# Kernel tuning notes

Hardware: AMD Instinct MI355X
Metric: run time of the kernel (lower is better)

Reference implementation:

```python
import jax, jax.numpy as jnp
import numpy as np

N = 100000   # nodes
E = 300000   # edges
D = 256      # emb_dim
L = 5        # num_layers
SELF_LOOP_BOND_TYPE = 4
BN_EPS = 1e-5


def setup_inputs() -> dict:
    key = jax.random.key(0)
    ks = jax.random.split(key, 12)
    s = 0.05
    x = jax.random.randint(ks[0], (N, 2), 0, 3)
    edge_index = jax.random.randint(ks[1], (2, E), 0, N)
    edge_attr = jax.random.randint(ks[2], (E, 2), 0, 3)
    x_emb1 = jax.random.normal(ks[3], (120, D), dtype=jnp.float32) * s
    x_emb2 = jax.random.normal(ks[4], (3, D), dtype=jnp.float32) * s
    edge_emb1 = jax.random.normal(ks[5], (L, 6, D), dtype=jnp.float32) * s
    edge_emb2 = jax.random.normal(ks[6], (L, 3, D), dtype=jnp.float32) * s
    W1 = jax.random.normal(ks[7], (L, D, 2 * D), dtype=jnp.float32) * (1.0 / np.sqrt(D))
    b1 = jnp.zeros((L, 2 * D), dtype=jnp.float32)
    W2 = jax.random.normal(ks[8], (L, 2 * D, D), dtype=jnp.float32) * (1.0 / np.sqrt(2 * D))
    b2 = jnp.zeros((L, D), dtype=jnp.float32)
    bn_gamma = jnp.ones((L - 1, D), dtype=jnp.float32)
    bn_beta = jnp.zeros((L - 1, D), dtype=jnp.float32)
    return dict(x=x, edge_index=edge_index, edge_attr=edge_attr,
                x_emb1=x_emb1, x_emb2=x_emb2,
                edge_emb1=edge_emb1, edge_emb2=edge_emb2,
                W1=W1, b1=b1, W2=W2, b2=b2,
                bn_gamma=bn_gamma, bn_beta=bn_beta)


def reference(x, edge_index, edge_attr, x_emb1, x_emb2, edge_emb1, edge_emb2,
              W1, b1, W2, b2, bn_gamma, bn_beta):
    n = x.shape[0]
    loop = jnp.arange(n)
    # add_self_loops: append (i, i) for every node
    src = jnp.concatenate([edge_index[0], loop])  # [E+N]
    dst = jnp.concatenate([edge_index[1], loop])  # [E+N]
    # self-loop edge_attr = (bond_type=4, direction=0)
    self_attr = jnp.concatenate([
        jnp.full((n, 1), SELF_LOOP_BOND_TYPE, dtype=edge_attr.dtype),
        jnp.zeros((n, 1), dtype=edge_attr.dtype)], axis=1)
    ea = jnp.concatenate([edge_attr, self_attr], axis=0)  # [E+N, 2]

    out = x_emb1[x[:, 0]] + x_emb2[x[:, 1]]  # [N, D]
    for l in range(L):
        e_emb = edge_emb1[l][ea[:, 0]] + edge_emb2[l][ea[:, 1]]  # [E+N, D]
        msg = out[src] + e_emb                                   # gather + message
        agg = jax.ops.segment_sum(msg, dst, num_segments=n)      # scatter-add
        h = jax.nn.relu(agg @ W1[l] + b1[l]) @ W2[l] + b2[l]     # GIN MLP
        if l < L - 1:
            mean = h.mean(axis=0)
            var = h.var(axis=0)  # biased var, matches torch BN training
            h = (h - mean) * jax.lax.rsqrt(var + BN_EPS) * bn_gamma[l] + bn_beta[l]
            h = jax.nn.relu(h)
        out = h
    return out
```

## Files before the change

### kernel.cpp

```cpp
#include <hip/hip_runtime.h>

typedef unsigned short u16;
typedef unsigned int u32;

#define DD 256

typedef short  s16x8 __attribute__((ext_vector_type(8)));
typedef short  s16x4 __attribute__((ext_vector_type(4)));
typedef float  f32x4 __attribute__((ext_vector_type(4)));

__device__ __forceinline__ float b2f(u16 u){
  union { u32 i; float f; } c; c.i = ((u32)u) << 16; return c.f;
}
__device__ __forceinline__ u16 f2b(float f){
  union { float f; u32 i; } c; c.f = f;
  u32 b = c.i + 0x7FFFu + ((c.i >> 16) & 1u);
  return (u16)(b >> 16);
}

__global__ void NodeEncoder_72971494359603_kernel(){}

__global__ void probe_dtype(const u32* w, u32* flag){
  if (threadIdx.x == 0 && blockIdx.x == 0){
    int cnt = 0;
    for (int i = 0; i < 256; i++){
      u32 low = w[i] & 0xFFFFu;
      u32 e = (low >> 7) & 0xFFu;
      if (e >= 0x60u && e <= 0x7Eu) cnt++;
    }
    *flag = (cnt >= 192) ? 1u : 0u;
  }
}

__global__ void cvt_in(const void* src, u16* dst, int n, const u32* flag){
  int i = blockIdx.x * 256 + threadIdx.x;
  if (i < n){
    if (*flag){
      dst[i] = ((const u16*)src)[i];
    } else {
      dst[i] = f2b(((const float*)src)[i]);
    }
  }
}

__global__ void store_out(const u16* h, void* dout, int n, const u32* flag){
  int i = blockIdx.x * 256 + threadIdx.x;
  if (i < n){
    if (*flag){
      ((u16*)dout)[i] = h[i];
    } else {
      ((float*)dout)[i] = b2f(h[i]);
    }
  }
}

__global__ void zero_int(int* p, int n){
  int i = blockIdx.x * 256 + threadIdx.x;
  if (i < n) p[i] = 0;
}

__global__ void build_table(const u16* ee1, const u16* ee2, u16* TBL){
  int b = blockIdx.x;
  int l = b / 18, c = b % 18, a = c / 3, bb = c % 3;
  int j = threadIdx.x;
  TBL[b * DD + j] = f2b(b2f(ee1[(l * 6 + a) * DD + j]) + b2f(ee2[(l * 3 + bb) * DD + j]));
}

__global__ void hist_kernel(const int* dst, int* counts, int E){
  int e = blockIdx.x * 256 + threadIdx.x;
  if (e < E) atomicAdd(&counts[dst[e]], 1);
}

__global__ void scan_sums(const int* counts, int* bsum, int N){
  __shared__ int red[256];
  int tid = threadIdx.x;
  int base = blockIdx.x * 1024;
  int s = 0;
  for (int i = tid; i < 1024; i += 256){
    int g = base + i;
    if (g < N) s += counts[g];
  }
  red[tid] = s;
  __syncthreads();
  for (int off = 128; off > 0; off >>= 1){
    if (tid < off) red[tid] += red[tid + off];
    __syncthreads();
  }
  if (tid == 0) bsum[blockIdx.x] = red[0];
}

__global__ void scan_top(int* bsum, int nb){
  if (threadIdx.x == 0 && blockIdx.x == 0){
    int acc = 0;
    for (int i = 0; i < nb; i++){ int t = bsum[i]; bsum[i] = acc; acc += t; }
  }
}

__global__ void scan_block(const int* counts, const int* bsum,
                           int* offsets, int* cursor, int N){
  __shared__ int tsum[256];
  int b = blockIdx.x;
  int tid = threadIdx.x;
  int base = b * 1024;
  int v0, v1, v2, v3;
  int g = base + tid * 4;
  v0 = (g + 0 < N) ? counts[g + 0] : 0;
  v1 = (g + 1 < N) ? counts[g + 1] : 0;
  v2 = (g + 2 < N) ? counts[g + 2] : 0;
  v3 = (g + 3 < N) ? counts[g + 3] : 0;
  tsum[tid] = v0 + v1 + v2 + v3;
  __syncthreads();
  for (int off = 1; off < 256; off <<= 1){
    int t = (tid >= off) ? tsum[tid - off] : 0;
    __syncthreads();
    tsum[tid] += t;
    __syncthreads();
  }
  int excl = (tid == 0 ? 0 : tsum[tid - 1]) + bsum[b];
  if (g + 0 < N){ offsets[g + 0] = excl; cursor[g + 0] = excl; } excl += v0;
  if (g + 1 < N){ offsets[g + 1] = excl; cursor[g + 1] = excl; } excl += v1;
  if (g + 2 < N){ offsets[g + 2] = excl; cursor[g + 2] = excl; } excl += v2;
  if (g + 3 < N){ offsets[g + 3] = excl; cursor[g + 3] = excl; }
}

__global__ void fill_csr(const int* ei, const int* ea, int* cursor,
                         int* payload, int E){
  int e = blockIdx.x * 256 + threadIdx.x;
  if (e < E){
    int d = ei[E + e];
    int pos = atomicAdd(&cursor[d], 1);
    int a = ea[2 * e], bb = ea[2 * e + 1];
    payload[pos] = ei[e] | ((a * 3 + bb) << 17);
  }
}

__global__ void node_embed(const int* x, const u16* xe1, const u16* xe2,
                           u16* out, int N){
  int idx = blockIdx.x * 256 + threadIdx.x;
  if (idx < N * DD){
    int n = idx >> 8, j = idx & 255;
    int x0 = x[2 * n], x1 = x[2 * n + 1];
    out[idx] = f2b(b2f(xe1[x0 * DD + j]) + b2f(xe2[x1 * DD + j]));
  }
}

__global__ void pack_B(const u16* __restrict__ W0, u16* __restrict__ Wp0, int K, int Nc){
  const u16* W = W0 + (size_t)blockIdx.y * K * Nc;
  u16* Wp = Wp0 + (size_t)blockIdx.y * K * Nc;
  int idx = blockIdx.x * 256 + threadIdx.x;
  int lane = idx & 63;
  int t = idx >> 6;
  int nk = K >> 5;
  int ksub = t % nk, cblk = t / nk;
  if (cblk >= (Nc >> 4)) return;
  int col = cblk * 16 + (lane & 15);
  int krow = ksub * 32 + (lane >> 4) * 8;
  u16* dst = Wp + (size_t)idx * 8;
#pragma unroll
  for (int e = 0; e < 8; e++)
    dst[e] = W[(size_t)(krow + e) * Nc + col];
}

__global__ __launch_bounds__(512, 6)
void layer_fused(const u16* __restrict__ feat, const u16* __restrict__ TBL,
                 const int* __restrict__ offsets, const int* __restrict__ counts,
                 const int* __restrict__ payload,
                 const u16* __restrict__ Wp1, const u16* __restrict__ bias1,
                 const u16* __restrict__ Wp2, const u16* __restrict__ bias2,
                 u16* __restrict__ H, float* __restrict__ partial, int npart, int M,
                 const float* __restrict__ sums, const u16* __restrict__ gamma,
                 const u16* __restrict__ beta, float invN, int apply_bn){
  __shared__ __align__(16) u16 As[64 * 256];
  __shared__ __align__(16) u16 Ms[2][64 * 64];
  u16* T = (u16*)Ms;
  int tid = threadIdx.x, lane = tid & 63, wave = tid >> 6;
  int wr = wave >> 2, wc = wave & 3;
  int row0 = blockIdx.x * 64;
  int lr = lane & 15, hi = lane >> 4;

  {
    u32* Tw = (u32*)T;
    const u32* Gw = (const u32*)TBL;
    for (int i = tid; i < 18 * DD / 2; i += 512) Tw[i] = Gw[i];
  }
  __syncthreads();

  {
    int c4 = lane * 4;
    float sc[4], sh[4];
    if (apply_bn){
#pragma unroll
      for (int e = 0; e < 4; e++){
        int j = c4 + e;
        float mean = sums[j] * invN;
        float var = sums[DD + j] * invN - mean * mean;
        if (var < 0.f) var = 0.f;
        float scl = rsqrtf(var + 1e-5f) * b2f(gamma[j]);
        sc[e] = scl; sh[e] = b2f(beta[j]) - mean * scl;
      }
    } else {
#pragma unroll
      for (int e = 0; e < 4; e++){ sc[e] = 1.f; sh[e] = 0.f; }
    }
    for (int u = 0; u < 8; u++){
      int r = wave * 8 + u;
      int n = row0 + r; if (n > M - 1) n = M - 1;
      s16x4 sv = *(const s16x4*)(feat + (size_t)n * DD + c4);
      s16x4 tb = *(const s16x4*)(T + 12 * DD + c4);
      float v0 = b2f((u16)sv[0]) * sc[0] + sh[0];
      float v1 = b2f((u16)sv[1]) * sc[1] + sh[1];
      float v2 = b2f((u16)sv[2]) * sc[2] + sh[2];
      float v3 = b2f((u16)sv[3]) * sc[3] + sh[3];
      if (apply_bn){
        v0 = fmaxf(v0, 0.f); v1 = fmaxf(v1, 0.f);
        v2 = fmaxf(v2, 0.f); v3 = fmaxf(v3, 0.f);
      }
      float a0 = v0 + b2f((u16)tb[0]);
      float a1 = v1 + b2f((u16)tb[1]);
      float a2 = v2 + b2f((u16)tb[2]);
      float a3 = v3 + b2f((u16)tb[3]);
      int e0 = offsets[n], eend = e0 + counts[n];
      for (int e = e0; e < eend; e += 4){
        int nb = eend - e; if (nb > 4) nb = 4;
        int pls[4]; s16x4 rvs[4]; s16x4 tvs[4];
#pragma unroll
        for (int i = 0; i < 4; i++)
          if (i < nb) pls[i] = payload[e + i];
#pragma unroll
        for (int i = 0; i < 4; i++)
          if (i < nb){
            rvs[i] = *(const s16x4*)(feat + (size_t)(pls[i] & 0x1FFFF) * DD + c4);
            tvs[i] = *(const s16x4*)(T + (pls[i] >> 17) * DD + c4);
          }
#pragma unroll
        for (int i = 0; i < 4; i++)
          if (i < nb){
            float w0 = b2f((u16)rvs[i][0]) * sc[0] + sh[0];
            float w1 = b2f((u16)rvs[i][1]) * sc[1] + sh[1];
            float w2 = b2f((u16)rvs[i][2]) * sc[2] + sh[2];
            float w3 = b2f((u16)rvs[i][3]) * sc[3] + sh[3];
            if (apply_bn){
              w0 = fmaxf(w0, 0.f); w1 = fmaxf(w1, 0.f);
              w2 = fmaxf(w2, 0.f); w3 = fmaxf(w3, 0.f);
            }
            a0 += w0 + b2f((u16)tvs[i][0]);
            a1 += w1 + b2f((u16)tvs[i][1]);
            a2 += w2 + b2f((u16)tvs[i][2]);
            a3 += w3 + b2f((u16)tvs[i][3]);
          }
      }
      s16x4 o;
      o[0] = (short)f2b(a0); o[1] = (short)f2b(a1);
      o[2] = (short)f2b(a2); o[3] = (short)f2b(a3);
      int byteo = r * 512 + ((((lane >> 1) ^ (r & 7)) & 31) << 4) + ((lane & 1) << 3);
      *(s16x4*)((char*)As + byteo) = o;
    }
  }
  __syncthreads();

  f32x4 zero = {0.f, 0.f, 0.f, 0.f};
  f32x4 acc2[2][4];
#pragma unroll
  for (int m = 0; m < 2; m++)
#pragma unroll
    for (int n = 0; n < 4; n++) acc2[m][n] = zero;
  f32x4 acc1[2];

  auto G1 = [&](int cc){
    acc1[0] = zero; acc1[1] = zero;
    int cb = cc * 4 + wc;
#pragma unroll
    for (int ks = 0; ks < 8; ks++){
      s16x8 af[2];
#pragma unroll
      for (int m = 0; m < 2; m++){
        int arow = wr * 32 + m * 16 + lr;
        af[m] = *(const s16x8*)((const char*)As + arow * 512 +
                                ((ks * 64 + hi * 16) ^ ((arow & 7) << 4)));
      }
      s16x8 bf = *(const s16x8*)(Wp1 + (((size_t)cb * 8 + ks) * 64 + lane) * 8);
      acc1[0] = __builtin_amdgcn_mfma_f32_16x16x32_bf16(af[0], bf, acc1[0], 0, 0, 0);
      acc1[1] = __builtin_amdgcn_mfma_f32_16x16x32_bf16(af[1], bf, acc1[1], 0, 0, 0);
    }
  };
  auto WMS = [&](int cc, int buf){
    char* ms = (char*)Ms[buf];
    float bv = b2f(bias1[cc * 64 + wc * 16 + lr]);
    int c2 = (wc * 16 + lr) * 2;
#pragma unroll
    for (int m = 0; m < 2; m++)
#pragma unroll
      for (int r = 0; r < 4; r++){
        int mrow = wr * 32 + m * 16 + hi * 4 + r;
        float v = fmaxf(acc1[m][r] + bv, 0.f);
        *(u16*)(ms + mrow * 128 + (c2 ^ ((mrow & 7) << 4))) = f2b(v);
      }
  };

  G1(0);
  WMS(0, 0);
  __syncthreads();

#pragma unroll
  for (int c = 0; c < 8; c++){
    const char* ms = (const char*)Ms[c & 1];
#pragma unroll
    for (int ks = 0; ks < 2; ks++){
      s16x8 mf[2];
#pragma unroll
      for (int m = 0; m < 2; m++){
        int mrow = wr * 32 + m * 16 + lr;
        mf[m] = *(const s16x8*)(ms + mrow * 128 +
                                ((ks * 64 + hi * 16) ^ ((mrow & 7) << 4)));
      }
#pragma unroll
      for (int n = 0; n < 4; n++){
        int cb2 = wc * 4 + n;
        s16x8 wf = *(const s16x8*)(Wp2 + (((size_t)cb2 * 16 + c * 2 + ks) * 64 + lane) * 8);
        acc2[0][n] = __builtin_amdgcn_mfma_f32_16x16x32_bf16(mf[0], wf, acc2[0][n], 0, 0, 0);
        acc2[1][n] = __builtin_amdgcn_mfma_f32_16x16x32_bf16(mf[1], wf, acc2[1][n], 0, 0, 0);
      }
    }
    if (c < 7){
      G1(c + 1);
      WMS(c + 1, (c + 1) & 1);
      __syncthreads();
    }
  }

#pragma unroll
  for (int n = 0; n < 4; n++){
    float bv = b2f(bias2[wc * 64 + n * 16 + lr]);
    int c2 = (wc * 64 + n * 16 + lr) * 2;
#pragma unroll
    for (int m = 0; m < 2; m++)
#pragma unroll
      for (int r = 0; r < 4; r++){
        int mrow = wr * 32 + m * 16 + hi * 4 + r;
        *(u16*)((char*)As + mrow * 512 + (c2 ^ ((mrow & 7) << 4))) = f2b(acc2[m][n][r] + bv);
      }
  }
  __syncthreads();

  float s[8], q[8];
#pragma unroll
  for (int e = 0; e < 8; e++){ s[e] = 0.f; q[e] = 0.f; }
  int sl = tid & 31;
#pragma unroll
  for (int p = 0; p < 4; p++){
    int r = p * 16 + (tid >> 5);
    s16x8 v = *(const s16x8*)((const char*)As + r * 512 + ((sl << 4) ^ ((r & 7) << 4)));
    int gr = row0 + r;
    if (gr < M){
      *(s16x8*)(H + (size_t)gr * DD + sl * 8) = v;
      if (partial){
#pragma unroll
        for (int e = 0; e < 8; e++){
          float f = b2f((u16)v[e]);
          s[e] += f; q[e] += f * f;
        }
      }
    }
  }
  if (partial){
#pragma unroll
    for (int e = 0; e < 8; e++){
      s[e] += __shfl_xor(s[e], 32);
      q[e] += __shfl_xor(q[e], 32);
    }
    __syncthreads();
    float* redS = (float*)Ms;
    float* redQ = redS + 8 * 256;
    if (lane < 32){
#pragma unroll
      for (int e = 0; e < 8; e++){
        redS[wave * 256 + sl * 8 + e] = s[e];
        redQ[wave * 256 + sl * 8 + e] = q[e];
      }
    }
    __syncthreads();
    if (tid < 256){
      float a = 0.f, b = 0.f;
#pragma unroll
      for (int w = 0; w < 8; w++){ a += redS[w * 256 + tid]; b += redQ[w * 256 + tid]; }
      partial[(size_t)blockIdx.x * DD + tid] = a;
      partial[(size_t)(npart + blockIdx.x) * DD + tid] = b;
    }
  }
}

__global__ void bn_reduce(const float* __restrict__ partial, float* __restrict__ sums,
                          int npart){
  int b = blockIdx.x, which = b >> 3, jg = b & 7;
  int t = threadIdx.x;
  int j = jg * 32 + (t >> 3);
  int li = t & 7;
  float s = 0.f;
  for (int i = li; i < npart; i += 8)
    s += partial[(size_t)(which * npart + i) * DD + j];
  s += __shfl_xor(s, 1); s += __shfl_xor(s, 2); s += __shfl_xor(s, 4);
  if (li == 0) sums[which * DD + j] = s;
}

extern "C" void kernel_launch(void* const* d_in, const int* in_sizes, int n_in,
                              void* d_out, int out_size, void* d_ws, size_t ws_size,
                              hipStream_t stream){
  (void)n_in; (void)out_size; (void)ws_size;
  const int* x    = (const int*)d_in[0];
  const int* ei   = (const int*)d_in[1];
  const int* ea   = (const int*)d_in[2];
  const void* xe1 = d_in[3];
  const void* xe2 = d_in[4];
  const void* ee1 = d_in[5];
  const void* ee2 = d_in[6];
  const void* W1  = d_in[7];
  const void* b1  = d_in[8];
  const void* W2  = d_in[9];
  const void* b2  = d_in[10];
  const void* gam = d_in[11];
  const void* bet = d_in[12];

  int N = in_sizes[0] / 2;
  int E = in_sizes[1] / 2;
  int NB = (N + 1023) / 1024;
  const int L = 5;
  int nblk = (N + 63) / 64;
  int npart = nblk;

  char* base = (char*)d_ws;
  size_t off = 0;
  u32* flag    = (u32*)(base + off);   off += 256;
  u16* TBL     = (u16*)(base + off);   off += ((size_t)L * 18 * DD * 2 + 255) & ~(size_t)255;
  int* counts  = (int*)(base + off);   off += ((size_t)N * 4 + 255) & ~(size_t)255;
  int* offsets = (int*)(base + off);   off += ((size_t)N * 4 + 255) & ~(size_t)255;
  int* cursor  = (int*)(base + off);   off += ((size_t)N * 4 + 255) & ~(size_t)255;
  int* bsum    = (int*)(base + off);   off += ((size_t)NB * 4 + 255) & ~(size_t)255;
  int* payload = (int*)(base + off);   off += ((size_t)E * 4 + 255) & ~(size_t)255;
  float* part  = (float*)(base + off); off += ((size_t)2 * npart * DD * 4 + 255) & ~(size_t)255;
  float* sums  = (float*)(base + off); off += ((size_t)2 * DD * 4 + 255) & ~(size_t)255;
  u16* wx1  = (u16*)(base + off); off += ((size_t)120 * DD * 2 + 255) & ~(size_t)255;
  u16* wx2  = (u16*)(base + off); off += ((size_t)3 * DD * 2 + 255) & ~(size_t)255;
  u16* wee1 = (u16*)(base + off); off += ((size_t)L * 6 * DD * 2 + 255) & ~(size_t)255;
  u16* wee2 = (u16*)(base + off); off += ((size_t)L * 3 * DD * 2 + 255) & ~(size_t)255;
  u16* wW1  = (u16*)(base + off); off += ((size_t)L * DD * 2 * DD * 2 + 255) & ~(size_t)255;
  u16* wb1  = (u16*)(base + off); off += ((size_t)L * 2 * DD * 2 + 255) & ~(size_t)255;
  u16* wW2  = (u16*)(base + off); off += ((size_t)L * 2 * DD * DD * 2 + 255) & ~(size_t)255;
  u16* wb2  = (u16*)(base + off); off += ((size_t)L * DD * 2 + 255) & ~(size_t)255;
  u16* wgam = (u16*)(base + off); off += ((size_t)(L - 1) * DD * 2 + 255) & ~(size_t)255;
  u16* wbet = (u16*)(base + off); off += ((size_t)(L - 1) * DD * 2 + 255) & ~(size_t)255;
  u16* Wp1  = (u16*)(base + off); off += ((size_t)L * DD * 2 * DD * 2 + 255) & ~(size_t)255;
  u16* Wp2  = (u16*)(base + off); off += ((size_t)L * 2 * DD * DD * 2 + 255) & ~(size_t)255;
  u16* featA = (u16*)(base + off); off += ((size_t)N * DD * 2 + 255) & ~(size_t)255;
  u16* featB = (u16*)(base + off); off += ((size_t)N * DD * 2 + 255) & ~(size_t)255;

  probe_dtype<<<1, 64, 0, stream>>>((const u32*)xe1, flag);
  cvt_in<<<(120 * DD + 255) / 256, 256, 0, stream>>>(xe1, wx1, 120 * DD, flag);
  cvt_in<<<(3 * DD + 255) / 256, 256, 0, stream>>>(xe2, wx2, 3 * DD, flag);
  cvt_in<<<(L * 6 * DD + 255) / 256, 256, 0, stream>>>(ee1, wee1, L * 6 * DD, flag);
  cvt_in<<<(L * 3 * DD + 255) / 256, 256, 0, stream>>>(ee2, wee2, L * 3 * DD, flag);
  cvt_in<<<(L * DD * 2 * DD + 255) / 256, 256, 0, stream>>>(W1, wW1, L * DD * 2 * DD, flag);
  cvt_in<<<(L * 2 * DD + 255) / 256, 256, 0, stream>>>(b1, wb1, L * 2 * DD, flag);
  cvt_in<<<(L * 2 * DD * DD + 255) / 256, 256, 0, stream>>>(W2, wW2, L * 2 * DD * DD, flag);
  cvt_in<<<(L * DD + 255) / 256, 256, 0, stream>>>(b2, wb2, L * DD, flag);
  cvt_in<<<((L - 1) * DD + 255) / 256, 256, 0, stream>>>(gam, wgam, (L - 1) * DD, flag);
  cvt_in<<<((L - 1) * DD + 255) / 256, 256, 0, stream>>>(bet, wbet, (L - 1) * DD, flag);

  build_table<<<90, 256, 0, stream>>>(wee1, wee2, TBL);
  pack_B<<<dim3(64, L), 256, 0, stream>>>(wW1, Wp1, DD, 2 * DD);
  pack_B<<<dim3(64, L), 256, 0, stream>>>(wW2, Wp2, 2 * DD, DD);
  zero_int<<<(N + 255) / 256, 256, 0, stream>>>(counts, N);
  hist_kernel<<<(E + 255) / 256, 256, 0, stream>>>(ei + E, counts, E);
  scan_sums<<<NB, 256, 0, stream>>>(counts, bsum, N);
  scan_top<<<1, 64, 0, stream>>>(bsum, NB);
  scan_block<<<NB, 256, 0, stream>>>(counts, bsum, offsets, cursor, N);
  fill_csr<<<(E + 255) / 256, 256, 0, stream>>>(ei, ea, cursor, payload, E);

  node_embed<<<(N * DD + 255) / 256, 256, 0, stream>>>(x, wx1, wx2, featA, N);

  float invN = 1.0f / (float)N;
  u16* fin = featA;
  u16* fout = featB;

  for (int l = 0; l < L; l++){
    layer_fused<<<nblk, 512, 0, stream>>>(
        fin, TBL + (size_t)l * 18 * DD, offsets, counts, payload,
        Wp1 + (size_t)l * DD * 2 * DD, wb1 + (size_t)l * 2 * DD,
        Wp2 + (size_t)l * 2 * DD * DD, wb2 + (size_t)l * DD,
        fout, (l < L - 1) ? part : (float*)nullptr, npart, N,
        sums, wgam + (size_t)(l > 0 ? l - 1 : 0) * DD,
        wbet + (size_t)(l > 0 ? l - 1 : 0) * DD, invN, l > 0 ? 1 : 0);

    if (l < L - 1){
      bn_reduce<<<16, 256, 0, stream>>>(part, sums, npart);
    }
    u16* t = fin; fin = fout; fout = t;
  }

  store_out<<<(N * DD + 255) / 256, 256, 0, stream>>>(fin, d_out, N * DD, flag);
}
```

Measured before the change: 1.573 ms.

## Switch fused GIN MLP to 32x32x16 MFMA tiles with wider swizzled LDS layout

```diff
diff --git a/kernel.cpp b/kernel.cpp
--- a/kernel.cpp
+++ b/kernel.cpp
@@ -8,6 +8,7 @@
 typedef short  s16x8 __attribute__((ext_vector_type(8)));
 typedef short  s16x4 __attribute__((ext_vector_type(4)));
 typedef float  f32x4 __attribute__((ext_vector_type(4)));
+typedef float  f32x16 __attribute__((ext_vector_type(16)));
 
 __device__ __forceinline__ float b2f(u16 u){
   union { u32 i; float f; } c; c.i = ((u32)u) << 16; return c.f;
@@ -150,18 +151,18 @@
   int idx = blockIdx.x * 256 + threadIdx.x;
   int lane = idx & 63;
   int t = idx >> 6;
-  int nk = K >> 5;
-  int ksub = t % nk, cblk = t / nk;
-  if (cblk >= (Nc >> 4)) return;
-  int col = cblk * 16 + (lane & 15);
-  int krow = ksub * 32 + (lane >> 4) * 8;
+  int nk = K >> 4;
+  int kstep = t % nk, cblk = t / nk;
+  if (cblk >= (Nc >> 5)) return;
+  int col = cblk * 32 + (lane & 31);
+  int krow = kstep * 16 + (lane >> 5) * 8;
   u16* dst = Wp + (size_t)idx * 8;
 #pragma unroll
   for (int e = 0; e < 8; e++)
     dst[e] = W[(size_t)(krow + e) * Nc + col];
 }
 
-__global__ __launch_bounds__(512, 6)
+__global__ __launch_bounds__(512, 4)
 void layer_fused(const u16* __restrict__ feat, const u16* __restrict__ TBL,
                  const int* __restrict__ offsets, const int* __restrict__ counts,
                  const int* __restrict__ payload,
@@ -171,12 +172,12 @@
                  const float* __restrict__ sums, const u16* __restrict__ gamma,
                  const u16* __restrict__ beta, float invN, int apply_bn){
   __shared__ __align__(16) u16 As[64 * 256];
-  __shared__ __align__(16) u16 Ms[2][64 * 64];
+  __shared__ __align__(16) u16 Ms[2][64 * 128];
   u16* T = (u16*)Ms;
   int tid = threadIdx.x, lane = tid & 63, wave = tid >> 6;
   int wr = wave >> 2, wc = wave & 3;
   int row0 = blockIdx.x * 64;
-  int lr = lane & 15, hi = lane >> 4;
+  int l31 = lane & 31, lhi = lane >> 5;
 
   {
     u32* Tw = (u32*)T;
@@ -252,49 +253,45 @@
       s16x4 o;
       o[0] = (short)f2b(a0); o[1] = (short)f2b(a1);
       o[2] = (short)f2b(a2); o[3] = (short)f2b(a3);
-      int byteo = r * 512 + ((((lane >> 1) ^ (r & 7)) & 31) << 4) + ((lane & 1) << 3);
+      int byteo = r * 512 + (((lane >> 1) ^ (r & 31)) << 4) + ((lane & 1) << 3);
       *(s16x4*)((char*)As + byteo) = o;
     }
   }
   __syncthreads();
 
-  f32x4 zero = {0.f, 0.f, 0.f, 0.f};
-  f32x4 acc2[2][4];
-#pragma unroll
-  for (int m = 0; m < 2; m++)
-#pragma unroll
-    for (int n = 0; n < 4; n++) acc2[m][n] = zero;
-  f32x4 acc1[2];
+  f32x16 acc2[2];
+#pragma unroll
+  for (int n = 0; n < 2; n++)
+#pragma unroll
+    for (int i = 0; i < 16; i++) acc2[n][i] = 0.f;
+  f32x16 acc1;
 
   auto G1 = [&](int cc){
-    acc1[0] = zero; acc1[1] = zero;
+    f32x16 a1;
+#pragma unroll
+    for (int i = 0; i < 16; i++) a1[i] = 0.f;
+    int arow = wr * 32 + l31;
     int cb = cc * 4 + wc;
 #pragma unroll
-    for (int ks = 0; ks < 8; ks++){
-      s16x8 af[2];
-#pragma unroll
-      for (int m = 0; m < 2; m++){
-        int arow = wr * 32 + m * 16 + lr;
-        af[m] = *(const s16x8*)((const char*)As + arow * 512 +
-                                ((ks * 64 + hi * 16) ^ ((arow & 7) << 4)));
-      }
-      s16x8 bf = *(const s16x8*)(Wp1 + (((size_t)cb * 8 + ks) * 64 + lane) * 8);
-      acc1[0] = __builtin_amdgcn_mfma_f32_16x16x32_bf16(af[0], bf, acc1[0], 0, 0, 0);
-      acc1[1] = __builtin_amdgcn_mfma_f32_16x16x32_bf16(af[1], bf, acc1[1], 0, 0, 0);
-    }
+    for (int ks = 0; ks < 16; ks++){
+      int slot = (ks * 2 + lhi) ^ (arow & 31);
+      s16x8 af = *(const s16x8*)((const char*)As + arow * 512 + (slot << 4));
+      s16x8 bf = *(const s16x8*)(Wp1 + (((size_t)cb * 16 + ks) * 64 + lane) * 8);
+      a1 = __builtin_amdgcn_mfma_f32_32x32x16_bf16(af, bf, a1, 0, 0, 0);
+    }
+    acc1 = a1;
   };
   auto WMS = [&](int cc, int buf){
     char* ms = (char*)Ms[buf];
-    float bv = b2f(bias1[cc * 64 + wc * 16 + lr]);
-    int c2 = (wc * 16 + lr) * 2;
-#pragma unroll
-    for (int m = 0; m < 2; m++)
-#pragma unroll
-      for (int r = 0; r < 4; r++){
-        int mrow = wr * 32 + m * 16 + hi * 4 + r;
-        float v = fmaxf(acc1[m][r] + bv, 0.f);
-        *(u16*)(ms + mrow * 128 + (c2 ^ ((mrow & 7) << 4))) = f2b(v);
-      }
+    int col = wc * 32 + l31;
+    float bv = b2f(bias1[cc * 128 + col]);
+#pragma unroll
+    for (int reg = 0; reg < 16; reg++){
+      int mrow = wr * 32 + (reg & 3) + 8 * (reg >> 2) + 4 * lhi;
+      float v = fmaxf(acc1[reg] + bv, 0.f);
+      int slot = (col >> 3) ^ (mrow & 15);
+      *(u16*)(ms + mrow * 256 + (slot << 4) + (col & 7) * 2) = f2b(v);
+    }
   };
 
   G1(0);
@@ -302,26 +299,21 @@
   __syncthreads();
 
 #pragma unroll
-  for (int c = 0; c < 8; c++){
+  for (int c = 0; c < 4; c++){
     const char* ms = (const char*)Ms[c & 1];
-#pragma unroll
-    for (int ks = 0; ks < 2; ks++){
-      s16x8 mf[2];
-#pragma unroll
-      for (int m = 0; m < 2; m++){
-        int mrow = wr * 32 + m * 16 + lr;
-        mf[m] = *(const s16x8*)(ms + mrow * 128 +
-                                ((ks * 64 + hi * 16) ^ ((mrow & 7) << 4)));
-      }
-#pragma unroll
-      for (int n = 0; n < 4; n++){
-        int cb2 = wc * 4 + n;
-        s16x8 wf = *(const s16x8*)(Wp2 + (((size_t)cb2 * 16 + c * 2 + ks) * 64 + lane) * 8);
-        acc2[0][n] = __builtin_amdgcn_mfma_f32_16x16x32_bf16(mf[0], wf, acc2[0][n], 0, 0, 0);
-        acc2[1][n] = __builtin_amdgcn_mfma_f32_16x16x32_bf16(mf[1], wf, acc2[1][n], 0, 0, 0);
-      }
-    }
-    if (c < 7){
+    int mrow = wr * 32 + l31;
+#pragma unroll
+    for (int ks = 0; ks < 8; ks++){
+      int slot = (ks * 2 + lhi) ^ (mrow & 15);
+      s16x8 mf = *(const s16x8*)(ms + mrow * 256 + (slot << 4));
+#pragma unroll
+      for (int n = 0; n < 2; n++){
+        int cb2 = wc * 2 + n;
+        s16x8 wf = *(const s16x8*)(Wp2 + (((size_t)cb2 * 32 + c * 8 + ks) * 64 + lane) * 8);
+        acc2[n] = __builtin_amdgcn_mfma_f32_32x32x16_bf16(mf, wf, acc2[n], 0, 0, 0);
+      }
+    }
+    if (c < 3){
       G1(c + 1);
       WMS(c + 1, (c + 1) & 1);
       __syncthreads();
@@ -329,16 +321,15 @@
   }
 
 #pragma unroll
-  for (int n = 0; n < 4; n++){
-    float bv = b2f(bias2[wc * 64 + n * 16 + lr]);
-    int c2 = (wc * 64 + n * 16 + lr) * 2;
-#pragma unroll
-    for (int m = 0; m < 2; m++)
-#pragma unroll
-      for (int r = 0; r < 4; r++){
-        int mrow = wr * 32 + m * 16 + hi * 4 + r;
-        *(u16*)((char*)As + mrow * 512 + (c2 ^ ((mrow & 7) << 4))) = f2b(acc2[m][n][r] + bv);
-      }
+  for (int n = 0; n < 2; n++){
+    int col = wc * 64 + n * 32 + l31;
+    float bv = b2f(bias2[col]);
+#pragma unroll
+    for (int reg = 0; reg < 16; reg++){
+      int row = wr * 32 + (reg & 3) + 8 * (reg >> 2) + 4 * lhi;
+      int slot = (col >> 3) ^ (row & 31);
+      *(u16*)((char*)As + row * 512 + (slot << 4) + (col & 7) * 2) = f2b(acc2[n][reg] + bv);
+    }
   }
   __syncthreads();
 
@@ -349,7 +340,7 @@
 #pragma unroll
   for (int p = 0; p < 4; p++){
     int r = p * 16 + (tid >> 5);
-    s16x8 v = *(const s16x8*)((const char*)As + r * 512 + ((sl << 4) ^ ((r & 7) << 4)));
+    s16x8 v = *(const s16x8*)((const char*)As + r * 512 + ((sl ^ (r & 31)) << 4));
     int gr = row0 + r;
     if (gr < M){
       *(s16x8*)(H + (size_t)gr * DD + sl * 8) = v;
```

Measured after the change: 1.604 ms. About the same (+1.9%).
